# Optimization experiments

Hardware: AMD Instinct MI355X
Metric: run time of the kernel (lower is better)

## Reference

```python
import jax, jax.numpy as jnp
import numpy as np

N_NODES = 40000
N_EDGES = 640000
IN_DIM = 7
HID = 128
N_LAYERS = 5


def setup_inputs() -> dict:
    key = jax.random.key(0)
    ks = jax.random.split(key, 12)
    x = jax.random.normal(ks[0], (N_NODES, IN_DIM), dtype=jnp.float32)
    edge_index = jax.random.randint(ks[1], (2, N_EDGES), 0, N_NODES, dtype=jnp.int64)
    # shift distances away from 0 so 1/d^2 weights stay finite across 5 layers
    dist = jax.random.uniform(ks[2], (N_EDGES,), dtype=jnp.float32) + 0.5
    s_enc = 1.0 / np.sqrt(IN_DIM)
    s_hid = 1.0 / np.sqrt(HID)
    enc_W = jax.random.normal(ks[3], (HID, IN_DIM), dtype=jnp.float32) * s_enc
    enc_b = jax.random.normal(ks[4], (HID,), dtype=jnp.float32) * 0.01
    conv_W = jax.random.normal(ks[5], (N_LAYERS, HID, HID), dtype=jnp.float32) * s_hid * 0.2
    conv_b = jax.random.normal(ks[6], (N_LAYERS, HID), dtype=jnp.float32) * 0.01
    cluster_W = jax.random.normal(ks[7], (3, HID), dtype=jnp.float32) * s_hid
    cluster_b = jax.random.normal(ks[8], (3,), dtype=jnp.float32) * 0.01
    energy_W = jax.random.normal(ks[9], (1, HID), dtype=jnp.float32) * s_hid
    energy_b = jax.random.normal(ks[10], (1,), dtype=jnp.float32) * 0.01
    return {"x": x, "edge_index": edge_index, "dist": dist,
            "enc_W": enc_W, "enc_b": enc_b,
            "conv_W": conv_W, "conv_b": conv_b,
            "cluster_W": cluster_W, "cluster_b": cluster_b,
            "energy_W": energy_W, "energy_b": energy_b}


def reference(x, edge_index, dist, enc_W, enc_b, conv_W, conv_b,
              cluster_W, cluster_b, energy_W, energy_b):
    n = x.shape[0]
    src = edge_index[0]  # x_j: source nodes (PyG source_to_target flow)
    dst = edge_index[1]  # aggregation target
    w = 1.0 / jnp.square(dist + 1e-6)  # [E]
    h = x @ enc_W.T + enc_b  # [N, H]
    for l in range(conv_W.shape[0]):
        # gather -> linear -> inverse-square weight -> scatter-add
        msg = (h[src] @ conv_W[l].T + conv_b[l]) * w[:, None]  # [E, H]
        h = jax.nn.relu(jax.ops.segment_sum(msg, dst, num_segments=n))
    cluster_probs = jax.nn.softmax(h @ cluster_W.T + cluster_b, axis=-1)  # [N, 3]
    energy = h.mean(axis=0, keepdims=True) @ energy_W.T + energy_b  # [1, 1]
    stable = energy < -1.0
    return cluster_probs, energy, stable
```

## Files before the change

kernel.cpp:

```cpp
#include <hip/hip_runtime.h>
#include <hip/hip_fp16.h>

#define NN 40000
#define NE 640000
#define HID 128
#define NL 5
#define NBLK 157
#define LSTRIDE 136

typedef __attribute__((ext_vector_type(8))) short bf16x8;
typedef __attribute__((ext_vector_type(4))) float f32x4;

static __device__ __forceinline__ unsigned short f32_to_bf16_rne(float f) {
  unsigned int u = __float_as_uint(f);
  unsigned int lsb = (u >> 16) & 1u;
  u += 0x7fffu + lsb;
  return (unsigned short)(u >> 16);
}
static __device__ __forceinline__ float bf16_to_f32(unsigned short s) {
  return __uint_as_float(((unsigned int)s) << 16);
}

__global__ void encoder_wconv_kernel(const float* __restrict__ x, const float* __restrict__ encW,
                                     const float* __restrict__ encb, __half* __restrict__ h,
                                     const float* __restrict__ convW,
                                     unsigned short* __restrict__ whi,
                                     unsigned short* __restrict__ wlo) {
  int b = blockIdx.x;
  if (b < 20000) {
    int gid = b * 256 + threadIdx.x;
    int n = gid >> 7, k = gid & 127;
    const float* xp = x + n * 7;
    const float* wp = encW + k * 7;
    float acc = encb[k];
#pragma unroll
    for (int i = 0; i < 7; ++i) acc += xp[i] * wp[i];
    h[gid] = __float2half(acc);
  } else {
    int i = (b - 20000) * 256 + threadIdx.x;
    if (i < NL * HID * HID) {
      float w = convW[i];
      unsigned short hi = f32_to_bf16_rne(w);
      unsigned short lo = f32_to_bf16_rne(w - bf16_to_f32(hi));
      whi[i] = hi;
      wlo[i] = lo;
    }
  }
}

__global__ void hist_kernel(const int* __restrict__ dst, int* __restrict__ cnt,
                            int* __restrict__ rank) {
  int e = blockIdx.x * blockDim.x + threadIdx.x;
  if (e < NE) rank[e] = atomicAdd(&cnt[dst[e]], 1);
}

__global__ void partial_kernel(const int* __restrict__ cnt, int* __restrict__ blocksum) {
  __shared__ int red[4];
  int t = threadIdx.x;
  int idx = blockIdx.x * 256 + t;
  int v = idx < NN ? cnt[idx] : 0;
#pragma unroll
  for (int off = 32; off > 0; off >>= 1) v += __shfl_xor(v, off, 64);
  if ((t & 63) == 0) red[t >> 6] = v;
  __syncthreads();
  if (t == 0) blocksum[blockIdx.x] = red[0] + red[1] + red[2] + red[3];
}

__global__ void scan_small_kernel(const int* __restrict__ blocksum, int* __restrict__ blockoff,
                                  int* __restrict__ row_ptr) {
  __shared__ int sh[256];
  int t = threadIdx.x;
  int v = t < NBLK ? blocksum[t] : 0;
  sh[t] = v;
  __syncthreads();
  for (int off = 1; off < 256; off <<= 1) {
    int u = (t >= off) ? sh[t - off] : 0;
    __syncthreads();
    sh[t] += u;
    __syncthreads();
  }
  if (t < NBLK) blockoff[t] = sh[t] - v;
  if (t == 255) row_ptr[NN] = sh[255];
}

__global__ void rowptr_kernel(const int* __restrict__ cnt, const int* __restrict__ blockoff,
                              int* __restrict__ row_ptr) {
  __shared__ int sh[256];
  int t = threadIdx.x;
  int idx = blockIdx.x * 256 + t;
  int v = idx < NN ? cnt[idx] : 0;
  sh[t] = v;
  __syncthreads();
  for (int off = 1; off < 256; off <<= 1) {
    int u = (t >= off) ? sh[t - off] : 0;
    __syncthreads();
    sh[t] += u;
    __syncthreads();
  }
  if (idx < NN) row_ptr[idx] = blockoff[blockIdx.x] + sh[t] - v;
}

__global__ void scatter_kernel(const int* __restrict__ src, const int* __restrict__ dst,
                               const float* __restrict__ dist,
                               const int* __restrict__ row_ptr, const int* __restrict__ rank,
                               int2* __restrict__ csr_ew) {
  int e = blockIdx.x * blockDim.x + threadIdx.x;
  if (e >= NE) return;
  int pos = row_ptr[dst[e]] + rank[e];
  float dd = dist[e] + 1e-6f;
  float w = 1.0f / (dd * dd);
  csr_ew[pos] = make_int2(src[e], (int)__float_as_uint(w));
}

__global__ void wsum_kernel(const int* __restrict__ row_ptr, const int2* __restrict__ csr_ew,
                            float* __restrict__ wsum) {
  int n = blockIdx.x * blockDim.x + threadIdx.x;
  if (n >= NN) return;
  int s = row_ptr[n], e = row_ptr[n + 1];
  float acc = 0.f;
  for (int i = s; i < e; ++i) acc += __uint_as_float((unsigned)csr_ew[i].y);
  wsum[n] = acc;
}

__global__ void __launch_bounds__(1024) fused_layer_kernel(
    const __half* __restrict__ hin, const int* __restrict__ row_ptr,
    const int2* __restrict__ csr_ew,
    const unsigned short* __restrict__ whi, const unsigned short* __restrict__ wlo,
    const float* __restrict__ wsum, const float* __restrict__ b,
    __half* __restrict__ hout) {
  __shared__ __align__(16) unsigned short sAh[16][LSTRIDE];
  __shared__ __align__(16) unsigned short sAl[16][LSTRIDE];
  int wave = threadIdx.x >> 6;
  int lane = threadIdx.x & 63;
  int wid = blockIdx.x * 16 + wave;

  {
    int s = __builtin_amdgcn_readfirstlane(row_ptr[wid]);
    int e = __builtin_amdgcn_readfirstlane(row_ptr[wid + 1]);
    int g = lane >> 4;
    int k = lane & 15;
    const __half* hp = hin + k * 8;
    float a[8] = {0.f, 0.f, 0.f, 0.f, 0.f, 0.f, 0.f, 0.f};
    int i = s;
    for (; i + 16 <= e; i += 16) {
      uint4 hv[4];
      float wv[4];
#pragma unroll
      for (int u = 0; u < 4; ++u) {
        int2 p = csr_ew[i + u * 4 + g];
        wv[u] = __uint_as_float((unsigned)p.y);
        hv[u] = *reinterpret_cast<const uint4*>(hp + (size_t)p.x * HID);
      }
#pragma unroll
      for (int u = 0; u < 4; ++u) {
        const __half2* q = reinterpret_cast<const __half2*>(&hv[u]);
#pragma unroll
        for (int c = 0; c < 4; ++c) {
          float2 f = __half22float2(q[c]);
          a[2 * c] += wv[u] * f.x;
          a[2 * c + 1] += wv[u] * f.y;
        }
      }
    }
    for (; i < e; i += 4) {
      int j = i + g;
      int jc = j < e ? j : e - 1;
      int2 p = csr_ew[jc];
      float w = (j < e) ? __uint_as_float((unsigned)p.y) : 0.f;
      uint4 hv = *reinterpret_cast<const uint4*>(hp + (size_t)p.x * HID);
      const __half2* q = reinterpret_cast<const __half2*>(&hv);
#pragma unroll
      for (int c = 0; c < 4; ++c) {
        float2 f = __half22float2(q[c]);
        a[2 * c] += w * f.x;
        a[2 * c + 1] += w * f.y;
      }
    }
#pragma unroll
    for (int c = 0; c < 8; ++c) {
      a[c] += __shfl_xor(a[c], 16, 64);
      a[c] += __shfl_xor(a[c], 32, 64);
    }
    if (g == 0) {
      unsigned short hh[8], ll[8];
#pragma unroll
      for (int c = 0; c < 8; ++c) {
        hh[c] = f32_to_bf16_rne(a[c]);
        ll[c] = f32_to_bf16_rne(a[c] - bf16_to_f32(hh[c]));
      }
      *reinterpret_cast<uint4*>(&sAh[wave][k * 8]) = *reinterpret_cast<const uint4*>(hh);
      *reinterpret_cast<uint4*>(&sAl[wave][k * 8]) = *reinterpret_cast<const uint4*>(ll);
    }
  }
  __syncthreads();

  if (wave >= 8) return;
  int t = wave;
  int mrow = lane & 15;
  int kc = (lane >> 4) * 8;

  f32x4 acc = (f32x4){0.f, 0.f, 0.f, 0.f};
#pragma unroll
  for (int si = 0; si < 4; ++si) {
    int joff = si * 32 + kc;
    bf16x8 ah = *reinterpret_cast<const bf16x8*>(&sAh[mrow][joff]);
    bf16x8 al = *reinterpret_cast<const bf16x8*>(&sAl[mrow][joff]);
    bf16x8 bh = *reinterpret_cast<const bf16x8*>(whi + (t * 16 + mrow) * HID + joff);
    bf16x8 bl = *reinterpret_cast<const bf16x8*>(wlo + (t * 16 + mrow) * HID + joff);
    acc = __builtin_amdgcn_mfma_f32_16x16x32_bf16(ah, bh, acc, 0, 0, 0);
    acc = __builtin_amdgcn_mfma_f32_16x16x32_bf16(ah, bl, acc, 0, 0, 0);
    acc = __builtin_amdgcn_mfma_f32_16x16x32_bf16(al, bh, acc, 0, 0, 0);
  }

  int nodeBase = blockIdx.x * 16 + (lane >> 4) * 4;
  int kout = t * 16 + mrow;
  float bk = b[kout];
#pragma unroll
  for (int r = 0; r < 4; ++r) {
    float v = acc[r] + bk * wsum[nodeBase + r];
    hout[(nodeBase + r) * HID + kout] = __float2half(fmaxf(v, 0.f));
  }
}

__global__ void cluster_kernel(const __half* __restrict__ h, const float* __restrict__ cW,
                               const float* __restrict__ cb, float* __restrict__ out) {
  int wid = (blockIdx.x * blockDim.x + threadIdx.x) >> 6;
  int lane = threadIdx.x & 63;
  if (wid >= NN) return;
  float h0 = __half2float(h[wid * HID + lane]);
  float h1 = __half2float(h[wid * HID + 64 + lane]);
  float logit[3];
#pragma unroll
  for (int c = 0; c < 3; ++c) {
    float p = h0 * cW[c * HID + lane] + h1 * cW[c * HID + 64 + lane];
#pragma unroll
    for (int off = 32; off > 0; off >>= 1) p += __shfl_xor(p, off, 64);
    logit[c] = p + cb[c];
  }
  if (lane == 0) {
    float m = fmaxf(logit[0], fmaxf(logit[1], logit[2]));
    float e0 = expf(logit[0] - m), e1 = expf(logit[1] - m), e2 = expf(logit[2] - m);
    float inv = 1.0f / (e0 + e1 + e2);
    out[wid * 3 + 0] = e0 * inv;
    out[wid * 3 + 1] = e1 * inv;
    out[wid * 3 + 2] = e2 * inv;
  }
}

__global__ void colsum_part_kernel(const __half* __restrict__ h, float* __restrict__ partial) {
  int t = threadIdx.x;
  int col = t & 127;
  int lane_id = blockIdx.x * 2 + (t >> 7);
  float acc = 0.f;
  for (int r = lane_id; r < NN; r += 2048) acc += __half2float(h[r * HID + col]);
  partial[lane_id * HID + col] = acc;
}

__global__ void energy_final_kernel(const float* __restrict__ partial,
                                    const float* __restrict__ eW, const float* __restrict__ eb,
                                    float* __restrict__ out) {
  __shared__ float sh[8][HID];
  __shared__ float red[2];
  int t = threadIdx.x;
  int col = t & 127;
  int slot = t >> 7;
  float acc = 0.f;
  for (int i = 0; i < 256; ++i) acc += partial[(slot + 8 * i) * HID + col];
  sh[slot][col] = acc;
  __syncthreads();
  if (t < 128) {
    float s = 0.f;
#pragma unroll
    for (int j = 0; j < 8; ++j) s += sh[j][t];
    float v = s * (1.0f / NN) * eW[t];
#pragma unroll
    for (int off = 32; off > 0; off >>= 1) v += __shfl_xor(v, off, 64);
    if ((t & 63) == 0) red[t >> 6] = v;
  }
  __syncthreads();
  if (t == 0) {
    float e = red[0] + red[1] + eb[0];
    out[NN * 3] = e;
    out[NN * 3 + 1] = (e < -1.0f) ? 1.0f : 0.0f;
  }
}

extern "C" void kernel_launch(void* const* d_in, const int* in_sizes, int n_in,
                              void* d_out, int out_size, void* d_ws, size_t ws_size,
                              hipStream_t stream) {
  const float* x    = (const float*)d_in[0];
  const int*   ei   = (const int*)d_in[1];
  const float* dist = (const float*)d_in[2];
  const float* encW = (const float*)d_in[3];
  const float* encb = (const float*)d_in[4];
  const float* convW = (const float*)d_in[5];
  const float* convb = (const float*)d_in[6];
  const float* cW   = (const float*)d_in[7];
  const float* cb   = (const float*)d_in[8];
  const float* eW   = (const float*)d_in[9];
  const float* eb   = (const float*)d_in[10];
  float* out = (float*)d_out;

  char* ws = (char*)d_ws;
  __half*         h1      = (__half*)        (ws + 0);
  __half*         h2      = (__half*)        (ws + 10240000);
  char*           scratch = (char*)          (ws + 20480000);
  int2*           csr_ew  = (int2*)          (ws + 30720000);
  int*            row_ptr = (int*)           (ws + 35840000);
  int*            cnt     = (int*)           (ws + 36000064);
  float*          wsum    = (float*)         (ws + 36160064);
  unsigned short* whi5    = (unsigned short*)(ws + 36320064);
  unsigned short* wlo5    = (unsigned short*)(ws + 36483904);
  int*            rank    = (int*)           (ws + 36647744);
  if (ws_size < (size_t)39207744) return;

  int*   blocksum = (int*)scratch;
  int*   blockoff = (int*)scratch + 512;
  float* partial  = (float*)scratch;

  const int* srcI = ei;
  const int* dstI = ei + NE;

  hipMemsetAsync(cnt, 0, 160000, stream);

  encoder_wconv_kernel<<<20320, 256, 0, stream>>>(x, encW, encb, h1, convW, whi5, wlo5);

  hist_kernel<<<(NE + 255) / 256, 256, 0, stream>>>(dstI, cnt, rank);
  partial_kernel<<<NBLK, 256, 0, stream>>>(cnt, blocksum);
  scan_small_kernel<<<1, 256, 0, stream>>>(blocksum, blockoff, row_ptr);
  rowptr_kernel<<<NBLK, 256, 0, stream>>>(cnt, blockoff, row_ptr);
  scatter_kernel<<<(NE + 255) / 256, 256, 0, stream>>>(srcI, dstI, dist, row_ptr, rank, csr_ew);
  wsum_kernel<<<(NN + 255) / 256, 256, 0, stream>>>(row_ptr, csr_ew, wsum);

  __half* hin = h1;
  __half* hout = h2;
  for (int l = 0; l < NL; ++l) {
    fused_layer_kernel<<<NN / 16, 1024, 0, stream>>>(hin, row_ptr, csr_ew,
                                                     whi5 + (size_t)l * HID * HID,
                                                     wlo5 + (size_t)l * HID * HID,
                                                     wsum, convb + (size_t)l * HID, hout);
    __half* tmp = hin; hin = hout; hout = tmp;
  }

  cluster_kernel<<<(NN * 64 + 255) / 256, 256, 0, stream>>>(hin, cW, cb, out);
  colsum_part_kernel<<<1024, 256, 0, stream>>>(hin, partial);
  energy_final_kernel<<<1, 1024, 0, stream>>>(partial, eW, eb, out);
}
```

Measured before the change: 331.1 us.

## Sort nodes by in-degree so each block processes similar-degree nodes

```diff
diff --git a/kernel.cpp b/kernel.cpp
--- a/kernel.cpp
+++ b/kernel.cpp
@@ -100,6 +100,41 @@
   if (idx < NN) row_ptr[idx] = blockoff[blockIdx.x] + sh[t] - v;
 }
 
+__global__ void dhist_kernel(const int* __restrict__ cnt, int* __restrict__ dbin) {
+  int n = blockIdx.x * 256 + threadIdx.x;
+  if (n < NN) {
+    int d = cnt[n];
+    if (d > 255) d = 255;
+    atomicAdd(&dbin[d], 1);
+  }
+}
+
+__global__ void dscan_kernel(const int* __restrict__ dbin, int* __restrict__ doff) {
+  __shared__ int sh[256];
+  int t = threadIdx.x;
+  int v = dbin[t];
+  sh[t] = v;
+  __syncthreads();
+  for (int off = 1; off < 256; off <<= 1) {
+    int u = (t >= off) ? sh[t - off] : 0;
+    __syncthreads();
+    sh[t] += u;
+    __syncthreads();
+  }
+  doff[t] = sh[t] - v;
+}
+
+__global__ void dperm_kernel(const int* __restrict__ cnt, const int* __restrict__ doff,
+                             int* __restrict__ dfill, int* __restrict__ perm) {
+  int n = blockIdx.x * 256 + threadIdx.x;
+  if (n < NN) {
+    int d = cnt[n];
+    if (d > 255) d = 255;
+    int pos = doff[d] + atomicAdd(&dfill[d], 1);
+    perm[pos] = n;
+  }
+}
+
 __global__ void scatter_kernel(const int* __restrict__ src, const int* __restrict__ dst,
                                const float* __restrict__ dist,
                                const int* __restrict__ row_ptr, const int* __restrict__ rank,
@@ -124,7 +159,7 @@
 
 __global__ void __launch_bounds__(1024) fused_layer_kernel(
     const __half* __restrict__ hin, const int* __restrict__ row_ptr,
-    const int2* __restrict__ csr_ew,
+    const int2* __restrict__ csr_ew, const int* __restrict__ perm,
     const unsigned short* __restrict__ whi, const unsigned short* __restrict__ wlo,
     const float* __restrict__ wsum, const float* __restrict__ b,
     __half* __restrict__ hout) {
@@ -132,7 +167,7 @@
   __shared__ __align__(16) unsigned short sAl[16][LSTRIDE];
   int wave = threadIdx.x >> 6;
   int lane = threadIdx.x & 63;
-  int wid = blockIdx.x * 16 + wave;
+  int wid = __builtin_amdgcn_readfirstlane(perm[blockIdx.x * 16 + wave]);
 
   {
     int s = __builtin_amdgcn_readfirstlane(row_ptr[wid]);
@@ -212,13 +247,14 @@
     acc = __builtin_amdgcn_mfma_f32_16x16x32_bf16(al, bh, acc, 0, 0, 0);
   }
 
-  int nodeBase = blockIdx.x * 16 + (lane >> 4) * 4;
+  int slotBase = (lane >> 4) * 4;
   int kout = t * 16 + mrow;
   float bk = b[kout];
 #pragma unroll
   for (int r = 0; r < 4; ++r) {
-    float v = acc[r] + bk * wsum[nodeBase + r];
-    hout[(nodeBase + r) * HID + kout] = __float2half(fmaxf(v, 0.f));
+    int node = perm[blockIdx.x * 16 + slotBase + r];
+    float v = acc[r] + bk * wsum[node];
+    hout[(size_t)node * HID + kout] = __float2half(fmaxf(v, 0.f));
   }
 }
 
@@ -312,16 +348,21 @@
   unsigned short* whi5    = (unsigned short*)(ws + 36320064);
   unsigned short* wlo5    = (unsigned short*)(ws + 36483904);
   int*            rank    = (int*)           (ws + 36647744);
-  if (ws_size < (size_t)39207744) return;
+  int*            perm    = (int*)           (ws + 39207744);
+  if (ws_size < (size_t)39367744) return;
 
   int*   blocksum = (int*)scratch;
   int*   blockoff = (int*)scratch + 512;
+  int*   dbin     = (int*)scratch + 1024;
+  int*   dfill    = (int*)scratch + 1280;
+  int*   doff     = (int*)scratch + 1536;
   float* partial  = (float*)scratch;
 
   const int* srcI = ei;
   const int* dstI = ei + NE;
 
   hipMemsetAsync(cnt, 0, 160000, stream);
+  hipMemsetAsync(dbin, 0, 2048, stream);
 
   encoder_wconv_kernel<<<20320, 256, 0, stream>>>(x, encW, encb, h1, convW, whi5, wlo5);
 
@@ -329,13 +370,16 @@
   partial_kernel<<<NBLK, 256, 0, stream>>>(cnt, blocksum);
   scan_small_kernel<<<1, 256, 0, stream>>>(blocksum, blockoff, row_ptr);
   rowptr_kernel<<<NBLK, 256, 0, stream>>>(cnt, blockoff, row_ptr);
+  dhist_kernel<<<NBLK, 256, 0, stream>>>(cnt, dbin);
+  dscan_kernel<<<1, 256, 0, stream>>>(dbin, doff);
+  dperm_kernel<<<NBLK, 256, 0, stream>>>(cnt, doff, dfill, perm);
   scatter_kernel<<<(NE + 255) / 256, 256, 0, stream>>>(srcI, dstI, dist, row_ptr, rank, csr_ew);
   wsum_kernel<<<(NN + 255) / 256, 256, 0, stream>>>(row_ptr, csr_ew, wsum);
 
   __half* hin = h1;
   __half* hout = h2;
   for (int l = 0; l < NL; ++l) {
-    fused_layer_kernel<<<NN / 16, 1024, 0, stream>>>(hin, row_ptr, csr_ew,
+    fused_layer_kernel<<<NN / 16, 1024, 0, stream>>>(hin, row_ptr, csr_ew, perm,
                                                      whi5 + (size_t)l * HID * HID,
                                                      wlo5 + (size_t)l * HID * HID,
                                                      wsum, convb + (size_t)l * HID, hout);
```

New measurement: 551.2 us. +66.4%, slower.
